# Optimization experiments

Measured on AMD Instinct MI355X. Metric: run time of the kernel, lower is better.

The kernel has to match this reference:

```python
import jax, jax.numpy as jnp
import numpy as np

EPS = 1e-5
NSEG = 2048  # batch.max()+1 with sorted_randint over [0, 2048)


def _bn(h, g, b, m, v):
    # eval-mode batch norm with running stats
    return (h - m) * jax.lax.rsqrt(v + EPS) * g + b


def _lin_params(key, fan_in, fan_out):
    kw, kb = jax.random.split(key)
    W = jax.random.normal(kw, (fan_out, fan_in), jnp.float32) / np.sqrt(fan_in)
    b = jax.random.normal(kb, (fan_out,), jnp.float32) * 0.01
    return W, b


def _bn_params(key, c):
    k1, k2, k3, k4 = jax.random.split(key, 4)
    g = 1.0 + 0.1 * jax.random.normal(k1, (c,), jnp.float32)
    be = 0.1 * jax.random.normal(k2, (c,), jnp.float32)
    m = 0.1 * jax.random.normal(k3, (c,), jnp.float32)
    v = jax.random.uniform(k4, (c,), jnp.float32, 0.5, 1.5)
    return g, be, m, v


def setup_inputs() -> dict:
    key = jax.random.key(0)
    ks = jax.random.split(key, 10)
    N, C, H, O = 500000, 128, 128, 64
    x = jax.random.normal(ks[0], (N, C), jnp.float32)
    batch = jnp.sort(jax.random.randint(ks[1], (N,), 0, NSEG)).astype(jnp.int32)
    W1, b1 = _lin_params(ks[2], C, H)
    W2, b2 = _lin_params(ks[3], H, H)
    W3, b3 = _lin_params(ks[4], H, H)
    Wo, bo = _lin_params(ks[5], 3 * H, O)
    g1, be1, m1, v1 = _bn_params(ks[6], H)
    g2, be2, m2, v2 = _bn_params(ks[7], H)
    g3, be3, m3, v3 = _bn_params(ks[8], H)
    go, beo, mo, vo = _bn_params(ks[9], O)
    return dict(x=x, batch=batch,
                W1=W1, b1=b1, g1=g1, be1=be1, m1=m1, v1=v1,
                W2=W2, b2=b2, g2=g2, be2=be2, m2=m2, v2=v2,
                W3=W3, b3=b3, g3=g3, be3=be3, m3=m3, v3=v3,
                Wo=Wo, bo=bo, go=go, beo=beo, mo=mo, vo=vo)


def reference(x, batch,
              W1, b1, g1, be1, m1, v1,
              W2, b2, g2, be2, m2, v2,
              W3, b3, g3, be3, m3, v3,
              Wo, bo, go, beo, mo, vo):
    h = jax.nn.relu(_bn(x @ W1.T + b1, g1, be1, m1, v1))
    h = jax.nn.relu(_bn(h @ W2.T + b2, g2, be2, m2, v2))
    h = jax.nn.relu(_bn(h @ W3.T + b3, g3, be3, m3, v3))  # (N, H)

    # fused segment sum / max / mean over batch ids
    sum_r = jax.ops.segment_sum(h, batch, num_segments=NSEG)          # (NSEG, H)
    cnt = jax.ops.segment_sum(jnp.ones((h.shape[0],), h.dtype), batch,
                              num_segments=NSEG)                      # (NSEG,)
    mean_r = sum_r / jnp.clip(cnt, 1.0)[:, None]
    max_r = jax.ops.segment_max(h, batch, num_segments=NSEG)
    max_r = jnp.where(cnt[:, None] > 0, max_r, 0.0)  # empty segments -> 0

    agg = jnp.concatenate([sum_r, max_r, mean_r], axis=-1)  # (NSEG, 3H)
    out = _bn(agg @ Wo.T + bo, go, beo, mo, vo)             # (NSEG, O)
    return out
```

## Files before the change

### kernel.cpp

```cpp
#include <hip/hip_runtime.h>

#define EPSF 1e-5f
#define NSEG 2048
#define NTHR 768
#define NWAVE 12
#define NBLK 256

typedef short s16x8 __attribute__((ext_vector_type(8)));
typedef float f32x16 __attribute__((ext_vector_type(16)));
typedef unsigned u32;

__device__ __forceinline__ u32 f2bfu(float f) {
  u32 u = __float_as_uint(f);
  u += 0x7FFFu + ((u >> 16) & 1u);
  return u >> 16;
}
__device__ __forceinline__ u32 pk2(float a, float b) {
  return f2bfu(a) | (f2bfu(b) << 16);
}
__device__ __forceinline__ u32 cvtpk(float a, float b) {
  u32 r;
  asm("v_cvt_pk_bf16_f32 %0, %1, %2" : "=v"(r) : "v"(a), "v"(b));
  return r;
}
__device__ __forceinline__ float bf2f(u32 h) {
  return __uint_as_float(h << 16);
}

union FragU { s16x8 v; u32 u[4]; };

struct LayerP { const float *W, *b, *g, *be, *m, *v; };

__global__ void zero_kernel(uint4* __restrict__ p, int n16) {
  int i = blockIdx.x * blockDim.x + threadIdx.x;
  if (i < n16) p[i] = make_uint4(0u, 0u, 0u, 0u);
}

__global__ void prep_kernel(LayerP p0, LayerP p1, LayerP p2,
                            unsigned short* __restrict__ wsW,
                            float* __restrict__ biasf) {
  const int L = blockIdx.x;
  LayerP p = (L == 0) ? p0 : ((L == 1) ? p1 : p2);
  const int t = threadIdx.x;
  uint2* wdst = (uint2*)(wsW + L * 16384);
  const float4* wsrc = (const float4*)p.W;
  for (int i = 0; i < 16; ++i) {
    int idx4 = t + i * 256;
    int c = idx4 >> 5;
    float s = p.g[c] * rsqrtf(p.v[c] + EPSF);
    float4 w = wsrc[idx4];
    wdst[idx4] = make_uint2(pk2(w.x * s, w.y * s), pk2(w.z * s, w.w * s));
  }
  if (t < 128) {
    float s = p.g[t] * rsqrtf(p.v[t] + EPSF);
    biasf[L * 128 + t] = p.b[t] * s + p.be[t] - p.m[t] * s;
  }
}

__global__ __launch_bounds__(NTHR, 3)
void enc_kernel(const float* __restrict__ x, const int* __restrict__ batch,
                const unsigned short* __restrict__ wsW, const float* __restrict__ biasf,
                float* __restrict__ seg_sum, int* __restrict__ seg_max,
                u32* __restrict__ seg_cnt, int N, int ntiles) {
  __shared__ __attribute__((aligned(16))) unsigned char lds[98304 + NWAVE * 4096];
  __shared__ __attribute__((aligned(16))) float bias_lds[384];
  const int t = threadIdx.x;
  const int lane = t & 63, wv = t >> 6;
  const int l31 = lane & 31, hi = lane >> 5;
  const int swz = l31 & 15;
  const int xaddr = (lane ^ 32) << 2;

  {
    const uint4* src = (const uint4*)wsW;
#pragma unroll
    for (int i = 0; i < 8; ++i) {
      int idx = t + i * NTHR;
      int byte = idx << 4;
      int dst = byte ^ (((byte >> 8) & 15) << 4);
      *(uint4*)&lds[dst] = src[idx];
    }
  }
  if (t < 384) bias_lds[t] = biasf[t];
  __syncthreads();

  float bias2[4];
#pragma unroll
  for (int cg = 0; cg < 4; ++cg) bias2[cg] = bias_lds[256 + cg * 32 + l31];

  const int hbase = 98304 + wv * 4096;
  const float4* x4 = (const float4*)x;

  const int w = blockIdx.x * NWAVE + wv;
  const int TW = NBLK * NWAVE;
  const int base = ntiles / TW, rem = ntiles % TW;
  const int t0 = w * base + (w < rem ? w : rem);
  const int t1 = t0 + base + (w < rem ? 1 : 0);

  for (int tile = t0; tile < t1; ++tile) {
    const bool full = (tile * 32 + 32 <= N);
    float4 xr[16];
    {
      const float4* xt = x4 + (size_t)tile * 1024 + lane;
#pragma unroll
      for (int i = 0; i < 16; ++i)
        xr[i] = full ? xt[i * 64] : make_float4(0.f, 0.f, 0.f, 0.f);
    }
    int rr = tile * 32 + l31;
    const int scur = (rr < N) ? batch[rr] : -1;

    FragU frag[8];
#pragma unroll
    for (int h = 0; h < 2; ++h) {
#pragma unroll
      for (int i = 0; i < 8; ++i) {
        int rowp = 2 * i + hi;
        float4 v = xr[8 * h + i];
        *(uint2*)&lds[hbase + rowp * 256 + ((((l31 >> 1) ^ rowp) << 4)) + (l31 & 1) * 8] =
            make_uint2(cvtpk(v.x, v.y), cvtpk(v.z, v.w));
      }
      if ((l31 >> 4) == h) {
        const int rowp = l31 & 15;
#pragma unroll
        for (int s = 0; s < 8; ++s)
          frag[s].v = *(const s16x8*)&lds[hbase + rowp * 256 + (((2 * s + hi) ^ rowp) << 4)];
      }
    }

    f32x16 accs[4];
#pragma unroll
    for (int L = 0; L < 3; ++L) {
      const int wb = L * 32768 + l31 * 256;
#pragma unroll
      for (int cg = 0; cg < 4; ++cg) {
        f32x16 z = {0,0,0,0,0,0,0,0,0,0,0,0,0,0,0,0};
        accs[cg] = z;
      }
#pragma unroll
      for (int s = 0; s < 8; ++s) {
#pragma unroll
        for (int cg = 0; cg < 4; ++cg) {
          const s16x8 a =
              *(const s16x8*)&lds[wb + cg * 8192 + (((2 * s + hi) ^ swz) << 4)];
          if (L < 2)
            accs[cg] = __builtin_amdgcn_mfma_f32_32x32x16_bf16(a, frag[s].v, accs[cg], 0, 0, 0);
          else
            accs[cg] = __builtin_amdgcn_mfma_f32_32x32x16_bf16(frag[s].v, a, accs[cg], 0, 0, 0);
        }
      }
      if (L < 2) {
#pragma unroll
        for (int cg = 0; cg < 4; ++cg) {
          float tr[16];
#pragma unroll
          for (int q = 0; q < 4; ++q) {
            int ch = cg * 32 + 4 * hi + 8 * q;
            const float4 bb = *(const float4*)&bias_lds[L * 128 + ch];
            tr[4 * q + 0] = fmaxf(accs[cg][4 * q + 0] + bb.x, 0.f);
            tr[4 * q + 1] = fmaxf(accs[cg][4 * q + 1] + bb.y, 0.f);
            tr[4 * q + 2] = fmaxf(accs[cg][4 * q + 2] + bb.z, 0.f);
            tr[4 * q + 3] = fmaxf(accs[cg][4 * q + 3] + bb.w, 0.f);
          }
#pragma unroll
          for (int kh = 0; kh < 2; ++kh) {
            u32 pw0 = cvtpk(tr[8 * kh + 0], tr[8 * kh + 1]);
            u32 pw1 = cvtpk(tr[8 * kh + 2], tr[8 * kh + 3]);
            u32 pu0 = cvtpk(tr[8 * kh + 4], tr[8 * kh + 5]);
            u32 pu1 = cvtpk(tr[8 * kh + 6], tr[8 * kh + 7]);
            u32 cw0 = (u32)__builtin_amdgcn_ds_bpermute(xaddr, (int)pw0);
            u32 cw1 = (u32)__builtin_amdgcn_ds_bpermute(xaddr, (int)pw1);
            u32 cu0 = (u32)__builtin_amdgcn_ds_bpermute(xaddr, (int)pu0);
            u32 cu1 = (u32)__builtin_amdgcn_ds_bpermute(xaddr, (int)pu1);
            frag[2 * cg + kh].u[0] = hi ? cu0 : pw0;
            frag[2 * cg + kh].u[1] = hi ? cu1 : pw1;
            frag[2 * cg + kh].u[2] = hi ? pu0 : cw0;
            frag[2 * cg + kh].u[3] = hi ? pu1 : cw1;
          }
        }
      }
    }

    const int nvalid = min(N - tile * 32, 32);
    const int sid0 = __builtin_amdgcn_readlane(scur, 0);
    const int sidL = __builtin_amdgcn_readlane(scur, nvalid - 1);
#pragma unroll
    for (int cg = 0; cg < 4; ++cg)
#pragma unroll
      for (int rg = 0; rg < 16; ++rg)
        accs[cg][rg] = fmaxf(accs[cg][rg] + bias2[cg], 0.f);

    if (nvalid == 32 && sid0 == sidL) {
#pragma unroll
      for (int cg = 0; cg < 4; ++cg) {
        float s = 0.f, mx = 0.f;
#pragma unroll
        for (int rg = 0; rg < 16; ++rg) { s += accs[cg][rg]; mx = fmaxf(mx, accs[cg][rg]); }
        float ps = __int_as_float(__builtin_amdgcn_ds_bpermute(xaddr, __float_as_int(s)));
        float pm = __int_as_float(__builtin_amdgcn_ds_bpermute(xaddr, __float_as_int(mx)));
        s += ps; mx = fmaxf(mx, pm);
        if (!hi) {
          atomicAdd(&seg_sum[sid0 * 128 + cg * 32 + l31], s);
          atomicMax(&seg_max[sid0 * 128 + cg * 32 + l31], __float_as_int(mx));
        }
      }
      if (lane == 0) atomicAdd(&seg_cnt[sid0], 32u);
    } else {
      int srow[16];
#pragma unroll
      for (int rg = 0; rg < 16; ++rg) {
        int m = (rg & 3) + 8 * (rg >> 2) + 4 * hi;
        srow[rg] = __builtin_amdgcn_ds_bpermute(m << 2, scur);
      }
      for (int sg = sid0; sg <= sidL; ++sg) {
#pragma unroll
        for (int cg = 0; cg < 4; ++cg) {
          float s = 0.f, mx = 0.f;
#pragma unroll
          for (int rg = 0; rg < 16; ++rg) {
            float v = (srow[rg] == sg) ? accs[cg][rg] : 0.f;
            s += v; mx = fmaxf(mx, v);
          }
          float ps = __int_as_float(__builtin_amdgcn_ds_bpermute(xaddr, __float_as_int(s)));
          float pm = __int_as_float(__builtin_amdgcn_ds_bpermute(xaddr, __float_as_int(mx)));
          s += ps; mx = fmaxf(mx, pm);
          if (!hi) {
            atomicAdd(&seg_sum[sg * 128 + cg * 32 + l31], s);
            atomicMax(&seg_max[sg * 128 + cg * 32 + l31], __float_as_int(mx));
          }
        }
        u32 c = (u32)__popcll(__ballot(hi == 0 && scur == sg));
        if (lane == 0) atomicAdd(&seg_cnt[sg], c);
      }
    }
  }
}

__global__ __launch_bounds__(128)
void proj_kernel(const float* __restrict__ seg_sum, const unsigned* __restrict__ seg_max,
                 const u32* __restrict__ seg_cnt,
                 const float* __restrict__ Wo, const float* __restrict__ bo,
                 const float* __restrict__ go, const float* __restrict__ beo,
                 const float* __restrict__ mo, const float* __restrict__ vo,
                 float* __restrict__ out) {
  __shared__ __attribute__((aligned(16))) float agg[384];
  __shared__ float part[64];
  const int s = blockIdx.x, t = threadIdx.x;
  float cinv = 1.f / fmaxf((float)seg_cnt[s], 1.f);
  for (int i = t; i < 384; i += 128) {
    float v;
    if (i < 128)      v = seg_sum[s * 128 + i];
    else if (i < 256) v = __uint_as_float(seg_max[s * 128 + i - 128]);
    else              v = seg_sum[s * 128 + i - 256] * cinv;
    agg[i] = v;
  }
  __syncthreads();
  const int o = t & 63, hf = t >> 6;
  const float4* wrow = (const float4*)(Wo + o * 384 + hf * 192);
  float acc = 0.f;
#pragma unroll 8
  for (int k4 = 0; k4 < 48; ++k4) {
    float4 w = wrow[k4];
    float4 a = *(const float4*)&agg[hf * 192 + k4 * 4];
    acc += w.x * a.x + w.y * a.y + w.z * a.z + w.w * a.w;
  }
  if (hf) part[o] = acc;
  __syncthreads();
  if (!hf) {
    acc += part[o];
    float sc = go[o] * rsqrtf(vo[o] + EPSF);
    out[s * 64 + o] = (acc + bo[o] - mo[o]) * sc + beo[o];
  }
}

extern "C" void kernel_launch(void* const* d_in, const int* in_sizes, int n_in,
                              void* d_out, int out_size, void* d_ws, size_t ws_size,
                              hipStream_t stream) {
  (void)n_in; (void)out_size; (void)ws_size;
  const float* x = (const float*)d_in[0];
  const int* batch = (const int*)d_in[1];
  LayerP P0{(const float*)d_in[2],  (const float*)d_in[3],  (const float*)d_in[4],
            (const float*)d_in[5],  (const float*)d_in[6],  (const float*)d_in[7]};
  LayerP P1{(const float*)d_in[8],  (const float*)d_in[9],  (const float*)d_in[10],
            (const float*)d_in[11], (const float*)d_in[12], (const float*)d_in[13]};
  LayerP P2{(const float*)d_in[14], (const float*)d_in[15], (const float*)d_in[16],
            (const float*)d_in[17], (const float*)d_in[18], (const float*)d_in[19]};
  const float* Wo  = (const float*)d_in[20];
  const float* bo  = (const float*)d_in[21];
  const float* go  = (const float*)d_in[22];
  const float* beo = (const float*)d_in[23];
  const float* mo  = (const float*)d_in[24];
  const float* vo  = (const float*)d_in[25];
  const int N = in_sizes[0] / 128;

  char* ws = (char*)d_ws;
  float* seg_sum = (float*)ws;
  int*   seg_max = (int*)(ws + (1u << 20));
  u32*   seg_cnt = (u32*)(ws + (2u << 20));
  unsigned short* wsW = (unsigned short*)(ws + (2u << 20) + 8192);
  float* biasf = (float*)(ws + (2u << 20) + 8192 + 98304);

  const int n16 = ((2 << 20) + 8192) / 16;
  zero_kernel<<<(n16 + 255) / 256, 256, 0, stream>>>((uint4*)d_ws, n16);
  prep_kernel<<<3, 256, 0, stream>>>(P0, P1, P2, wsW, biasf);
  const int ntiles = (N + 31) / 32;
  enc_kernel<<<NBLK, NTHR, 0, stream>>>(x, batch, wsW, biasf, seg_sum, seg_max, seg_cnt,
                                        N, ntiles);
  proj_kernel<<<NSEG, 128, 0, stream>>>(seg_sum, (const unsigned*)seg_max, seg_cnt,
                                        Wo, bo, go, beo, mo, vo, (float*)d_out);
}
```

Baseline: 114.1 us.

## Permute layer-2/3 weight K order to match MFMA accumulator layout, drop bpermutes

```diff
diff --git a/kernel.cpp b/kernel.cpp
--- a/kernel.cpp
+++ b/kernel.cpp
@@ -43,13 +43,24 @@
   LayerP p = (L == 0) ? p0 : ((L == 1) ? p1 : p2);
   const int t = threadIdx.x;
   uint2* wdst = (uint2*)(wsW + L * 16384);
-  const float4* wsrc = (const float4*)p.W;
-  for (int i = 0; i < 16; ++i) {
-    int idx4 = t + i * 256;
-    int c = idx4 >> 5;
-    float s = p.g[c] * rsqrtf(p.v[c] + EPSF);
-    float4 w = wsrc[idx4];
-    wdst[idx4] = make_uint2(pk2(w.x * s, w.y * s), pk2(w.z * s, w.w * s));
+  for (int i = 0; i < 8; ++i) {
+    int cid = t + i * 256;
+    int row = cid >> 4, ch = cid & 15;
+    float s = p.g[row] * rsqrtf(p.v[row] + EPSF);
+    float w[8];
+    if (L == 0) {
+      const float4* s4 = (const float4*)(p.W + row * 128 + ch * 8);
+      float4 a = s4[0], b = s4[1];
+      w[0]=a.x; w[1]=a.y; w[2]=a.z; w[3]=a.w; w[4]=b.x; w[5]=b.y; w[6]=b.z; w[7]=b.w;
+    } else {
+      int sp = ch >> 1, hi = ch & 1;
+      int kb = 32 * (sp >> 1) + 16 * (sp & 1) + 4 * hi;
+      const float* src = p.W + row * 128;
+      w[0]=src[kb+0]; w[1]=src[kb+1]; w[2]=src[kb+2];  w[3]=src[kb+3];
+      w[4]=src[kb+8]; w[5]=src[kb+9]; w[6]=src[kb+10]; w[7]=src[kb+11];
+    }
+    wdst[cid * 2 + 0] = make_uint2(pk2(w[0]*s, w[1]*s), pk2(w[2]*s, w[3]*s));
+    wdst[cid * 2 + 1] = make_uint2(pk2(w[4]*s, w[5]*s), pk2(w[6]*s, w[7]*s));
   }
   if (t < 128) {
     float s = p.g[t] * rsqrtf(p.v[t] + EPSF);
@@ -57,7 +68,7 @@
   }
 }
 
-__global__ __launch_bounds__(NTHR, 3)
+__global__ __launch_bounds__(NTHR) __attribute__((amdgpu_waves_per_eu(3, 3)))
 void enc_kernel(const float* __restrict__ x, const int* __restrict__ batch,
                 const unsigned short* __restrict__ wsW, const float* __restrict__ biasf,
                 float* __restrict__ seg_sum, int* __restrict__ seg_max,
@@ -162,18 +173,10 @@
           }
 #pragma unroll
           for (int kh = 0; kh < 2; ++kh) {
-            u32 pw0 = cvtpk(tr[8 * kh + 0], tr[8 * kh + 1]);
-            u32 pw1 = cvtpk(tr[8 * kh + 2], tr[8 * kh + 3]);
-            u32 pu0 = cvtpk(tr[8 * kh + 4], tr[8 * kh + 5]);
-            u32 pu1 = cvtpk(tr[8 * kh + 6], tr[8 * kh + 7]);
-            u32 cw0 = (u32)__builtin_amdgcn_ds_bpermute(xaddr, (int)pw0);
-            u32 cw1 = (u32)__builtin_amdgcn_ds_bpermute(xaddr, (int)pw1);
-            u32 cu0 = (u32)__builtin_amdgcn_ds_bpermute(xaddr, (int)pu0);
-            u32 cu1 = (u32)__builtin_amdgcn_ds_bpermute(xaddr, (int)pu1);
-            frag[2 * cg + kh].u[0] = hi ? cu0 : pw0;
-            frag[2 * cg + kh].u[1] = hi ? cu1 : pw1;
-            frag[2 * cg + kh].u[2] = hi ? pu0 : cw0;
-            frag[2 * cg + kh].u[3] = hi ? pu1 : cw1;
+            frag[2 * cg + kh].u[0] = cvtpk(tr[8 * kh + 0], tr[8 * kh + 1]);
+            frag[2 * cg + kh].u[1] = cvtpk(tr[8 * kh + 2], tr[8 * kh + 3]);
+            frag[2 * cg + kh].u[2] = cvtpk(tr[8 * kh + 4], tr[8 * kh + 5]);
+            frag[2 * cg + kh].u[3] = cvtpk(tr[8 * kh + 6], tr[8 * kh + 7]);
           }
         }
       }
```

Measured after the change: 109.8 us. 1.04x faster.
